# Kernel tuning notes

Measured on AMD Instinct MI355X. Metric: run time of the kernel, lower is better.

## Reference

```python
import jax, jax.numpy as jnp
import numpy as np
from jax import lax

# channel-gather index lists for the 16 c3 branches (from the torch source)
IDX3 = np.array([0,1,2, 1,2,3, 2,3,4, 3,4,5, 0,4,5, 0,1,5])          # 6 branches x 3 ch
IDX4 = np.array([0,1,2,3, 1,2,3,4, 2,3,4,5, 0,3,4,5, 0,1,4,5,
                 0,1,2,5, 0,1,3,4, 1,2,4,5, 0,2,3,5])                  # 9 branches x 4 ch
F6_SCALE = 1.7519


def _conv(x, w, groups=1):
    # NCHW x OIHW, stride 1, VALID padding (all convs in the model)
    return lax.conv_general_dilated(x, w, (1, 1), 'VALID', feature_group_count=groups)


def _avgpool2(x):
    return lax.reduce_window(x, 0.0, lax.add, (1, 1, 2, 2), (1, 1, 2, 2), 'VALID') * 0.25


def _bconv(x, w, b, groups=1):
    # BinaryConvFunction.forward: sign(conv(sign(x), sign(w)) + b)
    out = _conv(jnp.sign(x), jnp.sign(w), groups) + b[None, :, None, None]
    return jnp.sign(out)


def setup_inputs() -> dict:
    key = jax.random.key(0)
    ks = jax.random.split(key, 16)
    B = 8192
    return {
        'x':     jax.random.normal(ks[0], (B, 1, 32, 32), jnp.float32),
        'c1_w':  jax.random.normal(ks[1], (6, 1, 5, 5), jnp.float32) * 0.2,
        'c1_b':  jax.random.normal(ks[2], (6,), jnp.float32) * 0.1,
        'w3':    jax.random.normal(ks[3], (6, 3, 5, 5), jnp.float32),   # 6 grouped 3-ch branches
        'b3':    jax.random.normal(ks[4], (6,), jnp.float32) * 0.1,
        'w4':    jax.random.normal(ks[5], (9, 4, 5, 5), jnp.float32),   # 9 grouped 4-ch branches
        'b4':    jax.random.normal(ks[6], (9,), jnp.float32) * 0.1,
        'w6':    jax.random.normal(ks[7], (1, 6, 5, 5), jnp.float32),   # 1 branch on all 6 ch
        'b6':    jax.random.normal(ks[8], (1,), jnp.float32) * 0.1,
        'c5_w':  jax.random.normal(ks[9], (120, 16, 5, 5), jnp.float32),
        'c5_b':  jax.random.normal(ks[10], (120,), jnp.float32) * 0.1,
        'f6_w':  jax.random.normal(ks[11], (84, 120), jnp.float32) * 0.1,
        'f6_b':  jax.random.normal(ks[12], (84,), jnp.float32) * 0.1,
        'rbf_w': jax.random.normal(ks[13], (10, 84), jnp.float32) * 0.1,
        'rbf_b': jax.random.normal(ks[14], (10,), jnp.float32) * 0.1,
    }


def reference(x, c1_w, c1_b, w3, b3, w4, b4, w6, b6, c5_w, c5_b, f6_w, f6_b, rbf_w, rbf_b):
    # c1 (full-precision conv) + relu + s2 avgpool: [B,1,32,32] -> [B,6,14,14]
    h = _avgpool2(jax.nn.relu(_conv(x, c1_w) + c1_b[None, :, None, None]))
    # 16 binary branch convs, batched as grouped convs over gathered channels
    o3 = _bconv(h[:, IDX3], w3, b3, groups=6)   # [B,6,10,10]
    o4 = _bconv(h[:, IDX4], w4, b4, groups=9)   # [B,9,10,10]
    o6 = _bconv(h, w6, b6)                      # [B,1,10,10]
    h = jnp.concatenate([o3, o4, o6], axis=1)   # [B,16,10,10] (matches torch cat order)
    h = _avgpool2(jax.nn.relu(h))               # [B,16,5,5]
    h = _bconv(h, c5_w, c5_b)                   # [B,120,1,1]
    h = h.reshape(h.shape[0], -1)               # [B,120]
    h = jnp.tanh((h @ f6_w.T + f6_b) * F6_SCALE)
    return jax.nn.relu(h @ rbf_w.T + rbf_b)     # [B,10]
```

## Files before the change

### kernel.cpp

```cpp
#include <hip/hip_runtime.h>
#include <stdint.h>

constexpr int IDX3[18] = {0,1,2, 1,2,3, 2,3,4, 3,4,5, 0,4,5, 0,1,5};
constexpr int IDX4[36] = {0,1,2,3, 1,2,3,4, 2,3,4,5, 0,3,4,5, 0,1,4,5,
                          0,1,2,5, 0,1,3,4, 1,2,4,5, 0,2,3,5};


__global__ void prepack_kernel(const float* __restrict__ w3, const float* __restrict__ w4,
                               const float* __restrict__ w6, const float* __restrict__ c5w,
                               unsigned* __restrict__ ws) {
    int t = blockIdx.x * blockDim.x + threadIdx.x;
    if (t < 60) {
        const float* src = (t < 18) ? (w3 + t * 25)
                          : (t < 54) ? (w4 + (t - 18) * 25)
                          : (w6 + (t - 54) * 25);
        unsigned m = 0;
        for (int p = 0; p < 25; ++p) if (src[p] > 0.f) m |= 1u << p;
        ws[t] = m;
    } else if (t < 1620) {
        int q = t - 60, oc = q / 13, w = q % 13;
        unsigned m = 0;
        for (int b = 0; b < 32; ++b) {
            int g = w * 32 + b;
            int qi = g >> 4, ic = g & 15;
            if (qi < 25 && c5w[oc * 400 + ic * 25 + qi] > 0.f) m |= 1u << b;
        }
        ws[60 + q] = m;
    }
}

#define ROWS 36
#define IMGS 1156

__global__ __launch_bounds__(256, 4) void lenet_fused(
    const float* __restrict__ x, const float* __restrict__ c1w, const float* __restrict__ c1b,
    const float* __restrict__ b3, const float* __restrict__ b4, const float* __restrict__ b6,
    const float* __restrict__ c5b, const unsigned* __restrict__ ws,
    const float* __restrict__ f6w, const float* __restrict__ f6b,
    const float* __restrict__ rbfw, const float* __restrict__ rbfb,
    float* __restrict__ out, int B) {
    __shared__ float xs[3 * IMGS];
    __shared__ float wS[150];
    __shared__ float bS[6], b3S[6], b4S[9], b6S[1];
    __shared__ unsigned hrow[3][6][14];
    __shared__ unsigned sbits[3][100];
    __shared__ unsigned c5in[3][13];
    __shared__ unsigned h5[3][4];
    __shared__ float f6o[3][84];

    const int t = threadIdx.x;
    const int img0 = blockIdx.x * 3;
    const int nimg = min(3, B - img0);

    {
        const float4* src = (const float4*)(x + (size_t)img0 * 1024);
        for (int i = t; i < nimg * 256; i += 256) {
            int img = i >> 8, r = (i >> 3) & 31, q = i & 7;
            ((float4*)xs)[img * 289 + r * 9 + q] = src[i];
        }
    }
    if (t < 150) wS[t] = c1w[t];
    if (t < 6) { bS[t] = c1b[t]; b3S[t] = b3[t]; }
    if (t < 9) b4S[t] = b4[t];
    if (t == 0) b6S[0] = b6[0];
    if (t < 12) ((unsigned*)h5)[t] = 0;
    __syncthreads();

    if (t < nimg * 84) {
        const int denom = nimg * 6;
        int py = t / denom, rem = t % denom, img = rem / 6, c = rem % 6;
        float wr[25];
        #pragma unroll
        for (int i = 0; i < 25; ++i) wr[i] = wS[c * 25 + i];
        const float bias = bS[c];
        const float* xp = xs + img * IMGS + (2 * py) * ROWS;
        unsigned m = 0;
        #pragma unroll 1
        for (int ch = 0; ch < 7; ++ch) {
            float acc0[4], acc1[4];
            #pragma unroll
            for (int j = 0; j < 4; ++j) { acc0[j] = bias; acc1[j] = bias; }
            #pragma unroll
            for (int r = 0; r < 6; ++r) {
                const float4* rp = (const float4*)(xp + r * ROWS + 4 * ch);
                float4 va = rp[0];
                float4 vb = rp[1];
                float win[8] = {va.x, va.y, va.z, va.w, vb.x, vb.y, vb.z, vb.w};
                if (r <= 4) {
                    #pragma unroll
                    for (int kw = 0; kw < 5; ++kw) {
                        float wv = wr[r * 5 + kw];
                        #pragma unroll
                        for (int j = 0; j < 4; ++j) acc0[j] = fmaf(win[j + kw], wv, acc0[j]);
                    }
                }
                if (r >= 1) {
                    #pragma unroll
                    for (int kw = 0; kw < 5; ++kw) {
                        float wv = wr[(r - 1) * 5 + kw];
                        #pragma unroll
                        for (int j = 0; j < 4; ++j) acc1[j] = fmaf(win[j + kw], wv, acc1[j]);
                    }
                }
            }
            float m0 = fmaxf(fmaxf(acc0[0], acc0[1]), fmaxf(acc1[0], acc1[1]));
            float m1 = fmaxf(fmaxf(acc0[2], acc0[3]), fmaxf(acc1[2], acc1[3]));
            unsigned bits = (m0 > 0.f ? 1u : 0u) | (m1 > 0.f ? 2u : 0u);
            m |= bits << (2 * ch);
        }
        hrow[img][c][py] = m;
    }
    __syncthreads();

    for (int q = t; q < nimg * 100; q += 256) {
        int img = q / 100, p = q % 100, oy = p / 10, ox = p % 10;
        unsigned win[6];
        int wpop[6];
        #pragma unroll
        for (int c = 0; c < 6; ++c) {
            unsigned w = 0;
            #pragma unroll
            for (int r = 0; r < 5; ++r)
                w |= ((hrow[img][c][oy + r] >> ox) & 31u) << (5 * r);
            win[c] = w;
            wpop[c] = __popc(w);
        }
        unsigned m16 = 0;
        #pragma unroll
        for (int br = 0; br < 6; ++br) {
            int sum = 0, tot = 0;
            #pragma unroll
            for (int j = 0; j < 3; ++j) {
                int c = IDX3[br * 3 + j];
                tot += wpop[c];
                sum += __popc(win[c] & ws[br * 3 + j]);
            }
            if ((float)(2 * sum - tot) + b3S[br] > 0.f) m16 |= 1u << br;
        }
        #pragma unroll
        for (int br = 0; br < 9; ++br) {
            int sum = 0, tot = 0;
            #pragma unroll
            for (int j = 0; j < 4; ++j) {
                int c = IDX4[br * 4 + j];
                tot += wpop[c];
                sum += __popc(win[c] & ws[18 + br * 4 + j]);
            }
            if ((float)(2 * sum - tot) + b4S[br] > 0.f) m16 |= 1u << (6 + br);
        }
        {
            int sum = 0, tot = 0;
            #pragma unroll
            for (int c = 0; c < 6; ++c) {
                tot += wpop[c];
                sum += __popc(win[c] & ws[54 + c]);
            }
            if ((float)(2 * sum - tot) + b6S[0] > 0.f) m16 |= 1u << 15;
        }
        sbits[img][p] = m16;
    }
    __syncthreads();

    for (int q = t; q < nimg * 13; q += 256) {
        int img = q / 13, j = q % 13;
        int qi0 = 2 * j;
        int qy = qi0 / 5, qx = qi0 % 5, base = 2 * qy * 10 + 2 * qx;
        unsigned a0 = sbits[img][base] | sbits[img][base + 1] |
                      sbits[img][base + 10] | sbits[img][base + 11];
        unsigned word = a0 & 0xFFFFu;
        if (j < 12) {
            int qi1 = qi0 + 1;
            qy = qi1 / 5; qx = qi1 % 5; base = 2 * qy * 10 + 2 * qx;
            unsigned a1 = sbits[img][base] | sbits[img][base + 1] |
                          sbits[img][base + 10] | sbits[img][base + 11];
            word |= (a1 & 0xFFFFu) << 16;
        }
        c5in[img][j] = word;
    }
    __syncthreads();

    for (int q = t; q < nimg * 120; q += 256) {
        int img = q / 120, oc = q % 120;
        const unsigned* cm = ws + 60 + oc * 13;
        int sum = 0, tot = 0;
        #pragma unroll
        for (int w = 0; w < 13; ++w) {
            unsigned inw = c5in[img][w];
            tot += __popc(inw);
            sum += __popc(inw & cm[w]);
        }
        if ((float)(2 * sum - tot) + c5b[oc] > 0.f)
            atomicOr(&h5[img][oc >> 5], 1u << (oc & 31));
    }
    __syncthreads();

    if (t < nimg * 84) {
        int img = t / 84, j = t % 84;
        unsigned hw[4];
        #pragma unroll
        for (int w = 0; w < 4; ++w) hw[w] = h5[img][w];
        float acc = f6b[j];
        const float4* wrow = (const float4*)f6w + j * 30;
        #pragma unroll
        for (int kk = 0; kk < 30; ++kk) {
            float4 wv = wrow[kk];
            int k = 4 * kk;
            acc += ((hw[(k + 0) >> 5] >> ((k + 0) & 31)) & 1u) ? wv.x : -wv.x;
            acc += ((hw[(k + 1) >> 5] >> ((k + 1) & 31)) & 1u) ? wv.y : -wv.y;
            acc += ((hw[(k + 2) >> 5] >> ((k + 2) & 31)) & 1u) ? wv.z : -wv.z;
            acc += ((hw[(k + 3) >> 5] >> ((k + 3) & 31)) & 1u) ? wv.w : -wv.w;
        }
        f6o[img][j] = tanhf(1.7519f * acc);
    }
    __syncthreads();

    if (t < nimg * 10) {
        int img = t / 10, oc = t % 10;
        float sum = rbfb[oc];
        #pragma unroll 4
        for (int j = 0; j < 84; ++j) sum = fmaf(f6o[img][j], rbfw[oc * 84 + j], sum);
        out[(size_t)(img0 + img) * 10 + oc] = fmaxf(sum, 0.f);
    }
}

extern "C" void kernel_launch(void* const* d_in, const int* in_sizes, int n_in,
                              void* d_out, int out_size, void* d_ws, size_t ws_size,
                              hipStream_t stream) {
    const float* x    = (const float*)d_in[0];
    const float* c1w  = (const float*)d_in[1];
    const float* c1b  = (const float*)d_in[2];
    const float* w3   = (const float*)d_in[3];
    const float* b3   = (const float*)d_in[4];
    const float* w4   = (const float*)d_in[5];
    const float* b4   = (const float*)d_in[6];
    const float* w6   = (const float*)d_in[7];
    const float* b6   = (const float*)d_in[8];
    const float* c5w  = (const float*)d_in[9];
    const float* c5b  = (const float*)d_in[10];
    const float* f6w  = (const float*)d_in[11];
    const float* f6b  = (const float*)d_in[12];
    const float* rbfw = (const float*)d_in[13];
    const float* rbfb = (const float*)d_in[14];
    const int B = in_sizes[0] / 1024;

    unsigned* ws = (unsigned*)d_ws;

    prepack_kernel<<<dim3(7), dim3(256), 0, stream>>>(w3, w4, w6, c5w, ws);
    lenet_fused<<<dim3((B + 2) / 3), dim3(256), 0, stream>>>(
        x, c1w, c1b, b3, b4, b6, c5b, ws, f6w, f6b, rbfw, rbfb, (float*)d_out, B);
}
```

Baseline: 155.9 us.

## Shrink blocks to one wavefront over two images, using packed FMA and ballot-based c5

```diff
diff --git a/kernel.cpp b/kernel.cpp
--- a/kernel.cpp
+++ b/kernel.cpp
@@ -1,5 +1,7 @@
 #include <hip/hip_runtime.h>
 #include <stdint.h>
+
+typedef float v2f __attribute__((ext_vector_type(2)));
 
 constexpr int IDX3[18] = {0,1,2, 1,2,3, 2,3,4, 3,4,5, 0,4,5, 0,1,5};
 constexpr int IDX4[36] = {0,1,2,3, 1,2,3,4, 2,3,4,5, 0,3,4,5, 0,1,4,5,
@@ -32,79 +34,120 @@
 #define ROWS 36
 #define IMGS 1156
 
-__global__ __launch_bounds__(256, 4) void lenet_fused(
+__device__ __forceinline__ void c5_eval(const unsigned cw[13], int tot,
+                                        const unsigned* __restrict__ ws,
+                                        const float* __restrict__ c5b,
+                                        int lane, unsigned h5w[4]) {
+    {
+        const unsigned* cm = ws + 60 + lane * 13;
+        int sum = 0;
+        #pragma unroll
+        for (int w = 0; w < 13; ++w) sum += __popc(cw[w] & cm[w]);
+        bool pred = ((float)(2 * sum - tot) + c5b[lane]) > 0.f;
+        unsigned long long m = __ballot(pred);
+        h5w[0] = (unsigned)m;
+        h5w[1] = (unsigned)(m >> 32);
+    }
+    {
+        int oc = 64 + lane;
+        bool pred = false;
+        if (oc < 120) {
+            const unsigned* cm = ws + 60 + oc * 13;
+            int sum = 0;
+            #pragma unroll
+            for (int w = 0; w < 13; ++w) sum += __popc(cw[w] & cm[w]);
+            pred = ((float)(2 * sum - tot) + c5b[oc]) > 0.f;
+        }
+        unsigned long long m = __ballot(pred);
+        h5w[2] = (unsigned)m;
+        h5w[3] = (unsigned)(m >> 32);
+    }
+}
+
+__global__ __launch_bounds__(64) void lenet_fused(
     const float* __restrict__ x, const float* __restrict__ c1w, const float* __restrict__ c1b,
     const float* __restrict__ b3, const float* __restrict__ b4, const float* __restrict__ b6,
     const float* __restrict__ c5b, const unsigned* __restrict__ ws,
     const float* __restrict__ f6w, const float* __restrict__ f6b,
     const float* __restrict__ rbfw, const float* __restrict__ rbfb,
     float* __restrict__ out, int B) {
-    __shared__ float xs[3 * IMGS];
+    __shared__ float xs[2 * IMGS];
     __shared__ float wS[150];
     __shared__ float bS[6], b3S[6], b4S[9], b6S[1];
-    __shared__ unsigned hrow[3][6][14];
-    __shared__ unsigned sbits[3][100];
-    __shared__ unsigned c5in[3][13];
-    __shared__ unsigned h5[3][4];
-    __shared__ float f6o[3][84];
+    __shared__ unsigned hrow[2][6][14];
+    __shared__ unsigned sbits[2][100];
+    __shared__ unsigned c5in[2][13];
+    __shared__ float f6o[2][84];
 
     const int t = threadIdx.x;
-    const int img0 = blockIdx.x * 3;
-    const int nimg = min(3, B - img0);
+    const int img0 = blockIdx.x * 2;
+    const int nimg = min(2, B - img0);
 
     {
         const float4* src = (const float4*)(x + (size_t)img0 * 1024);
-        for (int i = t; i < nimg * 256; i += 256) {
+        for (int i = t; i < nimg * 256; i += 64) {
             int img = i >> 8, r = (i >> 3) & 31, q = i & 7;
             ((float4*)xs)[img * 289 + r * 9 + q] = src[i];
         }
     }
-    if (t < 150) wS[t] = c1w[t];
+    for (int i = t; i < 150; i += 64) wS[i] = c1w[i];
     if (t < 6) { bS[t] = c1b[t]; b3S[t] = b3[t]; }
     if (t < 9) b4S[t] = b4[t];
     if (t == 0) b6S[0] = b6[0];
-    if (t < 12) ((unsigned*)h5)[t] = 0;
-    __syncthreads();
-
-    if (t < nimg * 84) {
-        const int denom = nimg * 6;
-        int py = t / denom, rem = t % denom, img = rem / 6, c = rem % 6;
-        float wr[25];
-        #pragma unroll
-        for (int i = 0; i < 25; ++i) wr[i] = wS[c * 25 + i];
+    __syncthreads();
+
+    for (int q = t; q < 2 * 84; q += 64) {
+        int py = q / 12, rem = q % 12, img = rem / 6, c = rem % 6;
+        const float* wc = wS + c * 25;
+        float w0[5], w4r[5];
+        v2f wp[20];
+        #pragma unroll
+        for (int kw = 0; kw < 5; ++kw) { w0[kw] = wc[kw]; w4r[kw] = wc[20 + kw]; }
+        #pragma unroll
+        for (int r = 1; r <= 4; ++r)
+            #pragma unroll
+            for (int kw = 0; kw < 5; ++kw)
+                wp[(r - 1) * 5 + kw] = (v2f){wc[r * 5 + kw], wc[(r - 1) * 5 + kw]};
         const float bias = bS[c];
         const float* xp = xs + img * IMGS + (2 * py) * ROWS;
         unsigned m = 0;
         #pragma unroll 1
         for (int ch = 0; ch < 7; ++ch) {
-            float acc0[4], acc1[4];
-            #pragma unroll
-            for (int j = 0; j < 4; ++j) { acc0[j] = bias; acc1[j] = bias; }
+            v2f accp[4];
+            #pragma unroll
+            for (int j = 0; j < 4; ++j) accp[j] = (v2f){bias, bias};
             #pragma unroll
             for (int r = 0; r < 6; ++r) {
                 const float4* rp = (const float4*)(xp + r * ROWS + 4 * ch);
                 float4 va = rp[0];
                 float4 vb = rp[1];
                 float win[8] = {va.x, va.y, va.z, va.w, vb.x, vb.y, vb.z, vb.w};
-                if (r <= 4) {
+                if (r == 0) {
+                    #pragma unroll
+                    for (int kw = 0; kw < 5; ++kw)
+                        #pragma unroll
+                        for (int j = 0; j < 4; ++j)
+                            accp[j].x = fmaf(win[j + kw], w0[kw], accp[j].x);
+                } else if (r == 5) {
+                    #pragma unroll
+                    for (int kw = 0; kw < 5; ++kw)
+                        #pragma unroll
+                        for (int j = 0; j < 4; ++j)
+                            accp[j].y = fmaf(win[j + kw], w4r[kw], accp[j].y);
+                } else {
                     #pragma unroll
                     for (int kw = 0; kw < 5; ++kw) {
-                        float wv = wr[r * 5 + kw];
+                        v2f w2 = wp[(r - 1) * 5 + kw];
                         #pragma unroll
-                        for (int j = 0; j < 4; ++j) acc0[j] = fmaf(win[j + kw], wv, acc0[j]);
+                        for (int j = 0; j < 4; ++j) {
+                            v2f x2 = (v2f){win[j + kw], win[j + kw]};
+                            accp[j] = x2 * w2 + accp[j];
+                        }
                     }
                 }
-                if (r >= 1) {
-                    #pragma unroll
-                    for (int kw = 0; kw < 5; ++kw) {
-                        float wv = wr[(r - 1) * 5 + kw];
-                        #pragma unroll
-                        for (int j = 0; j < 4; ++j) acc1[j] = fmaf(win[j + kw], wv, acc1[j]);
-                    }
-                }
-            }
-            float m0 = fmaxf(fmaxf(acc0[0], acc0[1]), fmaxf(acc1[0], acc1[1]));
-            float m1 = fmaxf(fmaxf(acc0[2], acc0[3]), fmaxf(acc1[2], acc1[3]));
+            }
+            float m0 = fmaxf(fmaxf(accp[0].x, accp[0].y), fmaxf(accp[1].x, accp[1].y));
+            float m1 = fmaxf(fmaxf(accp[2].x, accp[2].y), fmaxf(accp[3].x, accp[3].y));
             unsigned bits = (m0 > 0.f ? 1u : 0u) | (m1 > 0.f ? 2u : 0u);
             m |= bits << (2 * ch);
         }
@@ -112,8 +155,8 @@
     }
     __syncthreads();
 
-    for (int q = t; q < nimg * 100; q += 256) {
-        int img = q / 100, p = q % 100, oy = p / 10, ox = p % 10;
+    for (int q = t; q < 2 * 100; q += 64) {
+        int img = (q >= 100) ? 1 : 0, p = q - img * 100, oy = p / 10, ox = p % 10;
         unsigned win[6];
         int wpop[6];
         #pragma unroll
@@ -161,8 +204,8 @@
     }
     __syncthreads();
 
-    for (int q = t; q < nimg * 13; q += 256) {
-        int img = q / 13, j = q % 13;
+    if (t < 2 * 13) {
+        int img = (t >= 13) ? 1 : 0, j = t - img * 13;
         int qi0 = 2 * j;
         int qy = qi0 / 5, qx = qi0 % 5, base = 2 * qy * 10 + 2 * qx;
         unsigned a0 = sbits[img][base] | sbits[img][base + 1] |
@@ -179,46 +222,59 @@
     }
     __syncthreads();
 
-    for (int q = t; q < nimg * 120; q += 256) {
-        int img = q / 120, oc = q % 120;
-        const unsigned* cm = ws + 60 + oc * 13;
-        int sum = 0, tot = 0;
-        #pragma unroll
-        for (int w = 0; w < 13; ++w) {
-            unsigned inw = c5in[img][w];
-            tot += __popc(inw);
-            sum += __popc(inw & cm[w]);
-        }
-        if ((float)(2 * sum - tot) + c5b[oc] > 0.f)
-            atomicOr(&h5[img][oc >> 5], 1u << (oc & 31));
-    }
-    __syncthreads();
-
-    if (t < nimg * 84) {
-        int img = t / 84, j = t % 84;
-        unsigned hw[4];
-        #pragma unroll
-        for (int w = 0; w < 4; ++w) hw[w] = h5[img][w];
-        float acc = f6b[j];
-        const float4* wrow = (const float4*)f6w + j * 30;
-        #pragma unroll
-        for (int kk = 0; kk < 30; ++kk) {
-            float4 wv = wrow[kk];
-            int k = 4 * kk;
-            acc += ((hw[(k + 0) >> 5] >> ((k + 0) & 31)) & 1u) ? wv.x : -wv.x;
-            acc += ((hw[(k + 1) >> 5] >> ((k + 1) & 31)) & 1u) ? wv.y : -wv.y;
-            acc += ((hw[(k + 2) >> 5] >> ((k + 2) & 31)) & 1u) ? wv.z : -wv.z;
-            acc += ((hw[(k + 3) >> 5] >> ((k + 3) & 31)) & 1u) ? wv.w : -wv.w;
-        }
-        f6o[img][j] = tanhf(1.7519f * acc);
+    unsigned h50[4], h51[4];
+    {
+        unsigned cw[13];
+        int tot = 0;
+        #pragma unroll
+        for (int w = 0; w < 13; ++w) { cw[w] = c5in[0][w]; tot += __popc(cw[w]); }
+        c5_eval(cw, tot, ws, c5b, t, h50);
+    }
+    {
+        unsigned cw[13];
+        int tot = 0;
+        #pragma unroll
+        for (int w = 0; w < 13; ++w) { cw[w] = c5in[1][w]; tot += __popc(cw[w]); }
+        c5_eval(cw, tot, ws, c5b, t, h51);
+    }
+
+    #pragma unroll 1
+    for (int jr = 0; jr < 2; ++jr) {
+        int j = jr * 64 + t;
+        if (j < 84) {
+            float a0 = f6b[j], a1 = a0;
+            const float4* wrow = (const float4*)f6w + j * 30;
+            #pragma unroll 5
+            for (int kk = 0; kk < 30; ++kk) {
+                float4 wv = wrow[kk];
+                float we[4] = {wv.x, wv.y, wv.z, wv.w};
+                #pragma unroll
+                for (int e = 0; e < 4; ++e) {
+                    int k = 4 * kk + e;
+                    float w = we[e];
+                    a0 += ((h50[k >> 5] >> (k & 31)) & 1u) ? w : -w;
+                    a1 += ((h51[k >> 5] >> (k & 31)) & 1u) ? w : -w;
+                }
+            }
+            f6o[0][j] = tanhf(1.7519f * a0);
+            f6o[1][j] = tanhf(1.7519f * a1);
+        }
     }
     __syncthreads();
 
     if (t < nimg * 10) {
-        int img = t / 10, oc = t % 10;
+        int img = (t >= 10) ? 1 : 0, oc = t - img * 10;
         float sum = rbfb[oc];
-        #pragma unroll 4
-        for (int j = 0; j < 84; ++j) sum = fmaf(f6o[img][j], rbfw[oc * 84 + j], sum);
+        const float4* rw = (const float4*)(rbfw + oc * 84);
+        #pragma unroll
+        for (int kk = 0; kk < 21; ++kk) {
+            float4 wv = rw[kk];
+            int j = 4 * kk;
+            sum = fmaf(f6o[img][j + 0], wv.x, sum);
+            sum = fmaf(f6o[img][j + 1], wv.y, sum);
+            sum = fmaf(f6o[img][j + 2], wv.z, sum);
+            sum = fmaf(f6o[img][j + 3], wv.w, sum);
+        }
         out[(size_t)(img0 + img) * 10 + oc] = fmaxf(sum, 0.f);
     }
 }
@@ -246,6 +302,6 @@
     unsigned* ws = (unsigned*)d_ws;
 
     prepack_kernel<<<dim3(7), dim3(256), 0, stream>>>(w3, w4, w6, c5w, ws);
-    lenet_fused<<<dim3((B + 2) / 3), dim3(256), 0, stream>>>(
+    lenet_fused<<<dim3((B + 1) / 2), dim3(64), 0, stream>>>(
         x, c1w, c1b, b3, b4, b6, c5b, ws, f6w, f6b, rbfw, rbfb, (float*)d_out, B);
 }
```

Result: slower. 175.3 us (+12.4%).
